# Kernel optimization log

Hardware: AMD Instinct MI355X
Metric: run time of the kernel (lower is better)

Reference implementation:

```python
import jax, jax.numpy as jnp
import numpy as np

B, S, D, H = 4, 1024, 256, 8  # batch, seq, d_model (== head_dim), n_heads
SCALE = 1.0 / float(np.sqrt(D))  # source references undefined self.scale; use 1/sqrt(d_model)


def setup_inputs() -> dict:
    key = jax.random.key(0)
    ks = jax.random.split(key, 11)
    w = 0.02
    return {
        "value_input": jax.random.normal(ks[0], (B, S, D), dtype=jnp.float32),
        "key_input": jax.random.normal(ks[1], (B, S, D), dtype=jnp.float32),
        "query_input": jax.random.normal(ks[2], (B, S, D), dtype=jnp.float32),
        "Wv": jax.random.normal(ks[3], (D, D * H), dtype=jnp.float32) * w,
        "bv": jnp.zeros((D * H,), dtype=jnp.float32),
        "Wk": jax.random.normal(ks[4], (D, D * H), dtype=jnp.float32) * w,
        "bk": jnp.zeros((D * H,), dtype=jnp.float32),
        "Wq": jax.random.normal(ks[5], (D, D * H), dtype=jnp.float32) * w,
        "bq": jnp.zeros((D * H,), dtype=jnp.float32),
        "Wo": jax.random.normal(ks[6], (D * H, D), dtype=jnp.float32) * w,
        "bo": jnp.zeros((D,), dtype=jnp.float32),
    }


def reference(value_input, key_input, query_input, Wv, bv, Wk, bk, Wq, bq, Wo, bo):
    # Fused QKV-style projections, then split into heads along last dim.
    # torch.split(..., d_model, dim=-1) == reshape to (B, S, H, D).
    v = (value_input @ Wv + bv).reshape(B, S, H, D)
    k = (key_input @ Wk + bk).reshape(B, S, H, D)
    q = (query_input @ Wq + bq).reshape(B, S, H, D)
    # Source: dot = k @ q^T  -> scores[b,h,key_pos,query_pos]
    scores = jnp.einsum('bkhd,bqhd->bhkq', k, q) * SCALE
    # Softmax over dim=-1 == the QUERY axis (faithful to source, nonstandard).
    attn = jax.nn.softmax(scores, axis=-1)
    # attn @ v : contract query axis with v's seq axis -> output indexed by key pos
    out_h = jnp.einsum('bhkq,bqhd->bkhd', attn, v)
    concat = out_h.reshape(B, S, H * D)
    return concat @ Wo + bo
```

## Files before the change

### kernel.cpp

```cpp
#include <hip/hip_runtime.h>
#include <cstddef>
#include <cstdint>

#define Bz 4
#define Sz 1024
#define Dm 256
#define Hh 8
#define DHh 2048
#define SCALE 0.0625f

typedef __attribute__((ext_vector_type(8))) short short8;
typedef __attribute__((ext_vector_type(16))) float f32x16;

__device__ inline unsigned short f2bf(float f){
  unsigned u = __float_as_uint(f);
  u += 0x7FFFu + ((u >> 16) & 1u);
  return (unsigned short)(u >> 16);
}
__device__ inline unsigned pk2(float a, float b){
  return (unsigned)f2bf(a) | ((unsigned)f2bf(b) << 16);
}
__device__ inline void gll16(const void* g, void* l){
  __builtin_amdgcn_global_load_lds((const __attribute__((address_space(1))) unsigned*)g,
                                   (__attribute__((address_space(3))) unsigned*)l, 16, 0, 0);
}
__device__ inline short8 lds8(const char* p){ return *(const short8*)p; }
__device__ inline f32x16 MM(short8 a, short8 b, f32x16 c){
  return __builtin_amdgcn_mfma_f32_32x32x16_bf16(a, b, c, 0, 0, 0);
}
__device__ inline f32x16 z16(){ f32x16 v; 
#pragma unroll
  for(int i=0;i<16;i++) v[i]=0.f; return v; }

__global__ __launch_bounds__(256) void cvt_bf16(const float* __restrict__ src,
                                                unsigned short* __restrict__ dst, int n4){
  int i = blockIdx.x*256 + threadIdx.x;
  if(i < n4){
    float4 v = ((const float4*)src)[i];
    ushort4 o; o.x=f2bf(v.x); o.y=f2bf(v.y); o.z=f2bf(v.z); o.w=f2bf(v.w);
    ((ushort4*)dst)[i] = o;
  }
}

__global__ __launch_bounds__(256) void cvt_transpose(const float* __restrict__ W,
    unsigned short* __restrict__ Wt, int K, int N){
  __shared__ float t[32][33];
  const int n0 = blockIdx.x*32, k0 = blockIdx.y*32;
  const int a = threadIdx.x >> 5, c = threadIdx.x & 31;
#pragma unroll
  for(int p=0;p<4;p++)
    t[a + p*8][c] = W[(size_t)(k0 + a + p*8)*N + n0 + c];
  __syncthreads();
#pragma unroll
  for(int p=0;p<4;p++)
    Wt[(size_t)(n0 + a + p*8)*K + k0 + c] = f2bf(t[c][a + p*8]);
}

template<int VAR>
__global__ __launch_bounds__(256) void gemm_proj(const unsigned short* __restrict__ A,
    const unsigned short* __restrict__ Bt, const float* __restrict__ bias,
    unsigned short* __restrict__ C){
  __shared__ __align__(16) char sm[32768];
  const int tid = threadIdx.x, w = tid>>6, lane = tid&63, l31 = lane&31, hp = lane>>5;
  const int wm = (w>>1)*64, wn = (w&1)*64;
  const int bm = blockIdx.y*128, bn = blockIdx.x*128;
  f32x16 acc[2][2]; acc[0][0]=z16(); acc[0][1]=z16(); acc[1][0]=z16(); acc[1][1]=z16();
  for(int kk=0; kk<256; kk+=64){
#pragma unroll
    for(int j=0;j<4;j++){
      int ci = (w*4+j)*64 + lane;
      int m = ci>>3, sl = ci&7;
      gll16(A  + (size_t)(bm+m)*256 + kk + ((sl ^ (m&7))<<3), sm + (w*4+j)*1024);
      gll16(Bt + (size_t)(bn+m)*256 + kk + ((sl ^ (m&7))<<3), sm + 16384 + (w*4+j)*1024);
    }
    __syncthreads();
#pragma unroll
    for(int s=0;s<4;s++){
      int m0 = wm + l31, m1 = wm + 32 + l31;
      int n0 = wn + l31, n1 = wn + 32 + l31;
      short8 a0 = lds8(sm + m0*128 + (((s*2+hp) ^ (m0&7))<<4));
      short8 a1 = lds8(sm + m1*128 + (((s*2+hp) ^ (m1&7))<<4));
      short8 b0 = lds8(sm + 16384 + n0*128 + (((s*2+hp) ^ (n0&7))<<4));
      short8 b1 = lds8(sm + 16384 + n1*128 + (((s*2+hp) ^ (n1&7))<<4));
      acc[0][0] = MM(a0,b0,acc[0][0]); acc[0][1] = MM(a0,b1,acc[0][1]);
      acc[1][0] = MM(a1,b0,acc[1][0]); acc[1][1] = MM(a1,b1,acc[1][1]);
    }
    __syncthreads();
  }
#pragma unroll
  for(int nh=0; nh<2; nh++){
    int ncol = bn + wn + nh*32 + l31;
    float bb = bias[ncol];
#pragma unroll
    for(int mh=0; mh<2; mh++){
      if(VAR == 2){
        int hidx = ncol >> 8, d = ncol & 255;
#pragma unroll
        for(int g=0; g<4; g++){
          int mrow = bm + wm + mh*32 + 8*g + 4*hp;
          int batch = mrow >> 10, sin = mrow & 1023;
          unsigned u0 = pk2(acc[mh][nh][4*g+0] + bb, acc[mh][nh][4*g+1] + bb);
          unsigned u1 = pk2(acc[mh][nh][4*g+2] + bb, acc[mh][nh][4*g+3] + bb);
          uint2 uu; uu.x = u0; uu.y = u1;
          *(uint2*)(C + ((size_t)((batch*Hh + hidx)*Dm + d))*Sz + sin) = uu;
        }
      } else {
#pragma unroll
        for(int r=0; r<16; r++){
          int mrow = bm + wm + mh*32 + (r&3) + 8*(r>>2) + 4*hp;
          float v = acc[mh][nh][r] + bb;
          if(VAR == 1) v *= SCALE;
          C[(size_t)mrow*DHh + ncol] = f2bf(v);
        }
      }
    }
  }
}

__global__ __launch_bounds__(512, 2) void attn_mfma(
    const unsigned short* __restrict__ Kp, const unsigned short* __restrict__ Qp,
    const unsigned short* __restrict__ Vt, unsigned short* __restrict__ Oc){
  __shared__ __align__(16) char sm[133120];
  const int tid = threadIdx.x, w = tid>>6, lane = tid&63, l31 = lane&31, hp = lane>>5;
  const int set = w>>2, ws = w&3;
  const int h = blockIdx.y, b = blockIdx.z;
  const int brow0 = blockIdx.x*128;
  const size_t vtbase = ((size_t)((b*Hh + h)*Dm))*Sz;

  short8 kp[16];
  {
    const unsigned short* kr = Kp + (size_t)(b*Sz + brow0 + ws*32 + l31)*DHh + h*Dm + hp*8;
#pragma unroll
    for(int ki=0; ki<16; ki++) kp[ki] = *(const short8*)(kr + ki*16);
  }
  f32x16 acc[8];
#pragma unroll
  for(int f=0; f<8; f++) acc[f] = z16();
  float m_run = -3.0e38f, l_run = 0.f;
  char* qpL = sm + set*16384;
  char* vtL = sm + 32768 + set*16384;

  for(int it=0; it<16; ++it){
    const int kv0 = set*512 + it*32;
#pragma unroll
    for(int j=0; j<4; j++){
      int ci = (ws*4+j)*64 + lane;
      int c = ci>>5, sl5 = ci&31;
      gll16(Qp + (size_t)(b*Sz + kv0 + c)*DHh + h*Dm + ((sl5 ^ (c&31))<<3),
            qpL + (ws*4+j)*1024);
      int dp = ci>>3, sv = (ci&7) ^ (dp&7);
      int d = dp*2 + (sv>>2), co = (sv&3)*8;
      gll16(Vt + vtbase + (size_t)d*Sz + kv0 + co, vtL + (ws*4+j)*1024);
    }
    __syncthreads();
    f32x16 S = z16();
#pragma unroll
    for(int ki=0; ki<16; ki++){
      short8 a = lds8(qpL + l31*512 + (((ki*2+hp) ^ (l31&31))<<4));
      S = MM(a, kp[ki], S);
    }
    float tmax = S[0];
#pragma unroll
    for(int r=1; r<16; r++) tmax = fmaxf(tmax, S[r]);
    tmax = fmaxf(tmax, __shfl_xor(tmax, 32));
    if(!__all(tmax <= m_run + 8.0f)){
      float mnew = fmaxf(m_run, tmax);
      float alpha = __expf(m_run - mnew);
      m_run = mnew; l_run *= alpha;
#pragma unroll
      for(int r=0; r<16; r++){
        int rr = (r&3) + 8*(r>>2) + 4*hp;
        float ar = __shfl(alpha, rr);
#pragma unroll
        for(int f=0; f<8; f++) acc[f][r] *= ar;
      }
    }
    float lsum = 0.f;
#pragma unroll
    for(int r=0; r<16; r++){ S[r] = __expf(S[r] - m_run); lsum += S[r]; }
    lsum += __shfl_xor(lsum, 32);
    l_run += lsum;
    short8 pa[2];
#pragma unroll
    for(int t=0; t<2; t++){
      unsigned w01 = pk2(S[t*8+0], S[t*8+1]);
      unsigned w23 = pk2(S[t*8+2], S[t*8+3]);
      unsigned w45 = pk2(S[t*8+4], S[t*8+5]);
      unsigned w67 = pk2(S[t*8+6], S[t*8+7]);
      unsigned x01 = __shfl_xor(w01, 32), x23 = __shfl_xor(w23, 32);
      unsigned x45 = __shfl_xor(w45, 32), x67 = __shfl_xor(w67, 32);
      union { unsigned u[4]; short8 s8; } U;
      if(hp == 0){ U.u[0]=w01; U.u[1]=w23; U.u[2]=x01; U.u[3]=x23; }
      else       { U.u[0]=x45; U.u[1]=x67; U.u[2]=w45; U.u[3]=w67; }
      pa[t] = U.s8;
    }
#pragma unroll
    for(int t=0; t<2; t++){
#pragma unroll
      for(int f=0; f<8; f++){
        int d = f*32 + l31;
        int dp = d>>1;
        int slot = (d&1)*4 + t*2 + hp;
        short8 vfr = lds8(vtL + dp*128 + ((slot ^ (dp&7))<<4));
        acc[f] = MM(pa[t], vfr, acc[f]);
      }
    }
    __syncthreads();
  }
  float* stats = (float*)(sm + 131072);
  if(lane < 32){ stats[(w*32 + lane)*2 + 0] = m_run; stats[(w*32 + lane)*2 + 1] = l_run; }
  __syncthreads();
  float* mg = (float*)sm + ws*8192;
  if(set == 1){
    float mA = stats[(ws*32 + l31)*2 + 0];
    float mf = fmaxf(mA, m_run);
    float bB = __expf(m_run - mf);
#pragma unroll
    for(int r=0; r<16; r++){
      int rr = (r&3) + 8*(r>>2) + 4*hp;
      float br = __shfl(bB, rr);
#pragma unroll
      for(int f=0; f<8; f++) mg[rr*256 + f*32 + l31] = acc[f][r]*br;
    }
  }
  __syncthreads();
  if(set == 0){
    float mB = stats[((4+ws)*32 + l31)*2 + 0];
    float lB = stats[((4+ws)*32 + l31)*2 + 1];
    float mf = fmaxf(m_run, mB);
    float bA = __expf(m_run - mf), bBv = __expf(mB - mf);
    float inv = 1.0f / (l_run*bA + lB*bBv);
#pragma unroll
    for(int r=0; r<16; r++){
      int rr = (r&3) + 8*(r>>2) + 4*hp;
      float bAr = __shfl(bA, rr);
      float invr = __shfl(inv, rr);
      int srow = brow0 + ws*32 + rr;
#pragma unroll
      for(int f=0; f<8; f++){
        float v = (acc[f][r]*bAr + mg[rr*256 + f*32 + l31]) * invr;
        Oc[(size_t)(b*Sz + srow)*DHh + h*Dm + f*32 + l31] = f2bf(v);
      }
    }
  }
}

__global__ __launch_bounds__(64) void gemm_out(const unsigned short* __restrict__ A,
    const unsigned short* __restrict__ Bt, const float* __restrict__ bias,
    float* __restrict__ C){
  __shared__ __align__(16) char sm[8192];
  const int lane = threadIdx.x, l31 = lane&31, hp = lane>>5;
  const int bm = blockIdx.y*32, bn = blockIdx.x*32;
  f32x16 acc = z16();
  for(int kk=0; kk<2048; kk+=64){
#pragma unroll
    for(int j=0; j<4; j++){
      int ci = j*64 + lane;
      int m = ci>>3, sl = ci&7;
      gll16(A  + (size_t)(bm+m)*DHh + kk + ((sl ^ (m&7))<<3), sm + j*1024);
      gll16(Bt + (size_t)(bn+m)*DHh + kk + ((sl ^ (m&7))<<3), sm + 4096 + j*1024);
    }
    __syncthreads();
#pragma unroll
    for(int s=0; s<4; s++){
      short8 a = lds8(sm + l31*128 + (((s*2+hp) ^ (l31&7))<<4));
      short8 b = lds8(sm + 4096 + l31*128 + (((s*2+hp) ^ (l31&7))<<4));
      acc = MM(a, b, acc);
    }
    __syncthreads();
  }
  float bb = bias[bn + l31];
#pragma unroll
  for(int r=0; r<16; r++){
    int mrow = bm + (r&3) + 8*(r>>2) + 4*hp;
    C[(size_t)mrow*Dm + bn + l31] = acc[r] + bb;
  }
}

extern "C" void kernel_launch(void* const* d_in, const int* in_sizes, int n_in,
                              void* d_out, int out_size, void* d_ws, size_t ws_size,
                              hipStream_t stream){
  (void)in_sizes; (void)n_in; (void)out_size; (void)ws_size;
  const float* value_in = (const float*)d_in[0];
  const float* key_in   = (const float*)d_in[1];
  const float* query_in = (const float*)d_in[2];
  const float* Wv = (const float*)d_in[3];
  const float* bv = (const float*)d_in[4];
  const float* Wk = (const float*)d_in[5];
  const float* bk = (const float*)d_in[6];
  const float* Wq = (const float*)d_in[7];
  const float* bq = (const float*)d_in[8];
  const float* Wo = (const float*)d_in[9];
  const float* bo = (const float*)d_in[10];

  char* ws = (char*)d_ws;
  unsigned short* av  = (unsigned short*)(ws + ((size_t) 0u<<20));
  unsigned short* ak  = (unsigned short*)(ws + ((size_t) 2u<<20));
  unsigned short* aq  = (unsigned short*)(ws + ((size_t) 4u<<20));
  unsigned short* wtv = (unsigned short*)(ws + ((size_t) 6u<<20));
  unsigned short* wtk = (unsigned short*)(ws + ((size_t) 7u<<20));
  unsigned short* wtq = (unsigned short*)(ws + ((size_t) 8u<<20));
  unsigned short* wto = (unsigned short*)(ws + ((size_t) 9u<<20));
  unsigned short* vt  = (unsigned short*)(ws + ((size_t)10u<<20));
  unsigned short* kb  = (unsigned short*)(ws + ((size_t)26u<<20));
  unsigned short* qb  = (unsigned short*)(ws + ((size_t)42u<<20));
  unsigned short* cc  = (unsigned short*)(ws + ((size_t)58u<<20));

  cvt_bf16<<<1024, 256, 0, stream>>>(value_in, av, 262144);
  cvt_bf16<<<1024, 256, 0, stream>>>(key_in,   ak, 262144);
  cvt_bf16<<<1024, 256, 0, stream>>>(query_in, aq, 262144);
  cvt_transpose<<<dim3(64, 8), 256, 0, stream>>>(Wv, wtv, 256, 2048);
  cvt_transpose<<<dim3(64, 8), 256, 0, stream>>>(Wk, wtk, 256, 2048);
  cvt_transpose<<<dim3(64, 8), 256, 0, stream>>>(Wq, wtq, 256, 2048);
  cvt_transpose<<<dim3(8, 64), 256, 0, stream>>>(Wo, wto, 2048, 256);

  gemm_proj<2><<<dim3(16, 32), 256, 0, stream>>>(av, wtv, bv, vt);
  gemm_proj<1><<<dim3(16, 32), 256, 0, stream>>>(ak, wtk, bk, kb);
  gemm_proj<0><<<dim3(16, 32), 256, 0, stream>>>(aq, wtq, bq, qb);

  attn_mfma<<<dim3(8, Hh, Bz), 512, 0, stream>>>(kb, qb, vt, cc);

  gemm_out<<<dim3(8, 128), 64, 0, stream>>>(cc, wto, bo, (float*)d_out);
}
```

Measured before the change: 251.3 us.

## Double-buffer LDS in GEMMs and attention, merge convert launches, retile output GEMM

```diff
diff --git a/kernel.cpp b/kernel.cpp
--- a/kernel.cpp
+++ b/kernel.cpp
@@ -28,24 +28,36 @@
 __device__ inline f32x16 MM(short8 a, short8 b, f32x16 c){
   return __builtin_amdgcn_mfma_f32_32x32x16_bf16(a, b, c, 0, 0, 0);
 }
-__device__ inline f32x16 z16(){ f32x16 v; 
+__device__ inline f32x16 z16(){ f32x16 v;
 #pragma unroll
   for(int i=0;i<16;i++) v[i]=0.f; return v; }
 
-__global__ __launch_bounds__(256) void cvt_bf16(const float* __restrict__ src,
-                                                unsigned short* __restrict__ dst, int n4){
-  int i = blockIdx.x*256 + threadIdx.x;
-  if(i < n4){
-    float4 v = ((const float4*)src)[i];
-    ushort4 o; o.x=f2bf(v.x); o.y=f2bf(v.y); o.z=f2bf(v.z); o.w=f2bf(v.w);
-    ((ushort4*)dst)[i] = o;
-  }
-}
-
-__global__ __launch_bounds__(256) void cvt_transpose(const float* __restrict__ W,
-    unsigned short* __restrict__ Wt, int K, int N){
+__global__ __launch_bounds__(256) void cvt_a(
+    const float* __restrict__ S0, const float* __restrict__ S1, const float* __restrict__ S2,
+    unsigned short* __restrict__ D0, unsigned short* __restrict__ D1, unsigned short* __restrict__ D2){
+  const int bx = blockIdx.x;
+  const int seg = bx >> 10;
+  const float* src = seg==0 ? S0 : seg==1 ? S1 : S2;
+  unsigned short* dst = seg==0 ? D0 : seg==1 ? D1 : D2;
+  const int i = (bx & 1023)*256 + threadIdx.x;
+  float4 v = ((const float4*)src)[i];
+  ushort4 o; o.x=f2bf(v.x); o.y=f2bf(v.y); o.z=f2bf(v.z); o.w=f2bf(v.w);
+  ((ushort4*)dst)[i] = o;
+}
+
+__global__ __launch_bounds__(256) void cvt_w(
+    const float* __restrict__ W0, const float* __restrict__ W1,
+    const float* __restrict__ W2, const float* __restrict__ W3,
+    unsigned short* __restrict__ T0, unsigned short* __restrict__ T1,
+    unsigned short* __restrict__ T2, unsigned short* __restrict__ T3){
   __shared__ float t[32][33];
-  const int n0 = blockIdx.x*32, k0 = blockIdx.y*32;
+  const int z = blockIdx.z;
+  const float* W = z==0 ? W0 : z==1 ? W1 : z==2 ? W2 : W3;
+  unsigned short* T = z==0 ? T0 : z==1 ? T1 : z==2 ? T2 : T3;
+  const int K = (z<3) ? 256 : 2048;
+  const int N = (z<3) ? 2048 : 256;
+  const int n0 = (z<3) ? blockIdx.x*32 : blockIdx.y*32;
+  const int k0 = (z<3) ? blockIdx.y*32 : blockIdx.x*32;
   const int a = threadIdx.x >> 5, c = threadIdx.x & 31;
 #pragma unroll
   for(int p=0;p<4;p++)
@@ -53,39 +65,48 @@
   __syncthreads();
 #pragma unroll
   for(int p=0;p<4;p++)
-    Wt[(size_t)(n0 + a + p*8)*K + k0 + c] = f2bf(t[c][a + p*8]);
+    T[(size_t)(n0 + a + p*8)*K + k0 + c] = f2bf(t[c][a + p*8]);
 }
 
 template<int VAR>
 __global__ __launch_bounds__(256) void gemm_proj(const unsigned short* __restrict__ A,
     const unsigned short* __restrict__ Bt, const float* __restrict__ bias,
     unsigned short* __restrict__ C){
-  __shared__ __align__(16) char sm[32768];
+  __shared__ __align__(16) char sm[65536];
   const int tid = threadIdx.x, w = tid>>6, lane = tid&63, l31 = lane&31, hp = lane>>5;
   const int wm = (w>>1)*64, wn = (w&1)*64;
   const int bm = blockIdx.y*128, bn = blockIdx.x*128;
   f32x16 acc[2][2]; acc[0][0]=z16(); acc[0][1]=z16(); acc[1][0]=z16(); acc[1][1]=z16();
-  for(int kk=0; kk<256; kk+=64){
+
+  auto STAGE = [&](int db, int kk){
 #pragma unroll
     for(int j=0;j<4;j++){
       int ci = (w*4+j)*64 + lane;
       int m = ci>>3, sl = ci&7;
-      gll16(A  + (size_t)(bm+m)*256 + kk + ((sl ^ (m&7))<<3), sm + (w*4+j)*1024);
-      gll16(Bt + (size_t)(bn+m)*256 + kk + ((sl ^ (m&7))<<3), sm + 16384 + (w*4+j)*1024);
-    }
-    __syncthreads();
+      gll16(A  + (size_t)(bm+m)*256 + kk + ((sl ^ (m&7))<<3), sm + db*32768 + (w*4+j)*1024);
+      gll16(Bt + (size_t)(bn+m)*256 + kk + ((sl ^ (m&7))<<3), sm + db*32768 + 16384 + (w*4+j)*1024);
+    }
+  };
+
+  STAGE(0, 0);
+  __syncthreads();
+  int db = 0;
+  for(int t=0; t<4; ++t){
+    if(t<3) STAGE(db^1, (t+1)*64);
+    const char* base = sm + db*32768;
 #pragma unroll
     for(int s=0;s<4;s++){
       int m0 = wm + l31, m1 = wm + 32 + l31;
       int n0 = wn + l31, n1 = wn + 32 + l31;
-      short8 a0 = lds8(sm + m0*128 + (((s*2+hp) ^ (m0&7))<<4));
-      short8 a1 = lds8(sm + m1*128 + (((s*2+hp) ^ (m1&7))<<4));
-      short8 b0 = lds8(sm + 16384 + n0*128 + (((s*2+hp) ^ (n0&7))<<4));
-      short8 b1 = lds8(sm + 16384 + n1*128 + (((s*2+hp) ^ (n1&7))<<4));
+      short8 a0 = lds8(base + m0*128 + (((s*2+hp) ^ (m0&7))<<4));
+      short8 a1 = lds8(base + m1*128 + (((s*2+hp) ^ (m1&7))<<4));
+      short8 b0 = lds8(base + 16384 + n0*128 + (((s*2+hp) ^ (n0&7))<<4));
+      short8 b1 = lds8(base + 16384 + n1*128 + (((s*2+hp) ^ (n1&7))<<4));
       acc[0][0] = MM(a0,b0,acc[0][0]); acc[0][1] = MM(a0,b1,acc[0][1]);
       acc[1][0] = MM(a1,b0,acc[1][0]); acc[1][1] = MM(a1,b1,acc[1][1]);
     }
     __syncthreads();
+    db ^= 1;
   }
 #pragma unroll
   for(int nh=0; nh<2; nh++){
@@ -123,8 +144,10 @@
   __shared__ __align__(16) char sm[133120];
   const int tid = threadIdx.x, w = tid>>6, lane = tid&63, l31 = lane&31, hp = lane>>5;
   const int set = w>>2, ws = w&3;
-  const int h = blockIdx.y, b = blockIdx.z;
-  const int brow0 = blockIdx.x*128;
+  const int bid = blockIdx.x;
+  const int g = (bid & 7)*4 + (bid >> 6);
+  const int b = g >> 3, h = g & 7;
+  const int brow0 = ((bid >> 3) & 7) * 128;
   const size_t vtbase = ((size_t)((b*Hh + h)*Dm))*Sz;
 
   short8 kp[16];
@@ -137,26 +160,34 @@
 #pragma unroll
   for(int f=0; f<8; f++) acc[f] = z16();
   float m_run = -3.0e38f, l_run = 0.f;
-  char* qpL = sm + set*16384;
-  char* vtL = sm + 32768 + set*16384;
-
-  for(int it=0; it<16; ++it){
+
+  auto STAGE = [&](int db, int it){
     const int kv0 = set*512 + it*32;
+    char* qpD = sm + db*65536 + set*16384;
+    char* vtD = sm + db*65536 + 32768 + set*16384;
 #pragma unroll
     for(int j=0; j<4; j++){
       int ci = (ws*4+j)*64 + lane;
       int c = ci>>5, sl5 = ci&31;
-      gll16(Qp + (size_t)(b*Sz + kv0 + c)*DHh + h*Dm + ((sl5 ^ (c&31))<<3),
-            qpL + (ws*4+j)*1024);
+      gll16(Qp + (size_t)(b*Sz + kv0 + c)*DHh + h*Dm + ((sl5 ^ c)<<3),
+            qpD + (ws*4+j)*1024);
       int dp = ci>>3, sv = (ci&7) ^ (dp&7);
       int d = dp*2 + (sv>>2), co = (sv&3)*8;
-      gll16(Vt + vtbase + (size_t)d*Sz + kv0 + co, vtL + (ws*4+j)*1024);
-    }
-    __syncthreads();
+      gll16(Vt + vtbase + (size_t)d*Sz + kv0 + co, vtD + (ws*4+j)*1024);
+    }
+  };
+
+  STAGE(0, 0);
+  __syncthreads();
+  int db = 0;
+  for(int it=0; it<16; ++it){
+    if(it<15) STAGE(db^1, it+1);
+    const char* qpL = sm + db*65536 + set*16384;
+    const char* vtL = sm + db*65536 + 32768 + set*16384;
     f32x16 S = z16();
 #pragma unroll
     for(int ki=0; ki<16; ki++){
-      short8 a = lds8(qpL + l31*512 + (((ki*2+hp) ^ (l31&31))<<4));
+      short8 a = lds8(qpL + l31*512 + (((ki*2+hp) ^ l31)<<4));
       S = MM(a, kp[ki], S);
     }
     float tmax = S[0];
@@ -206,6 +237,7 @@
       }
     }
     __syncthreads();
+    db ^= 1;
   }
   float* stats = (float*)(sm + 131072);
   if(lane < 32){ stats[(w*32 + lane)*2 + 0] = m_run; stats[(w*32 + lane)*2 + 1] = l_run; }
@@ -245,35 +277,46 @@
   }
 }
 
-__global__ __launch_bounds__(64) void gemm_out(const unsigned short* __restrict__ A,
+__global__ __launch_bounds__(256) void gemm_out(const unsigned short* __restrict__ A,
     const unsigned short* __restrict__ Bt, const float* __restrict__ bias,
     float* __restrict__ C){
-  __shared__ __align__(16) char sm[8192];
-  const int lane = threadIdx.x, l31 = lane&31, hp = lane>>5;
-  const int bm = blockIdx.y*32, bn = blockIdx.x*32;
+  __shared__ __align__(16) char sm[32768];
+  const int tid = threadIdx.x, w = tid>>6, lane = tid&63, l31 = lane&31, hp = lane>>5;
+  const int wm = (w>>1)*32, wn = (w&1)*32;
+  const int bm = blockIdx.y*64, bn = blockIdx.x*64;
   f32x16 acc = z16();
-  for(int kk=0; kk<2048; kk+=64){
-#pragma unroll
-    for(int j=0; j<4; j++){
-      int ci = j*64 + lane;
+
+  auto STAGE = [&](int db, int kk){
+#pragma unroll
+    for(int j=0; j<2; j++){
+      int ci = (w*2+j)*64 + lane;
       int m = ci>>3, sl = ci&7;
-      gll16(A  + (size_t)(bm+m)*DHh + kk + ((sl ^ (m&7))<<3), sm + j*1024);
-      gll16(Bt + (size_t)(bn+m)*DHh + kk + ((sl ^ (m&7))<<3), sm + 4096 + j*1024);
+      gll16(A  + (size_t)(bm+m)*DHh + kk + ((sl ^ (m&7))<<3), sm + db*16384 + (w*2+j)*1024);
+      gll16(Bt + (size_t)(bn+m)*DHh + kk + ((sl ^ (m&7))<<3), sm + db*16384 + 8192 + (w*2+j)*1024);
+    }
+  };
+
+  STAGE(0, 0);
+  __syncthreads();
+  int db = 0;
+  for(int t=0; t<32; ++t){
+    if(t<31) STAGE(db^1, (t+1)*64);
+    const char* base = sm + db*16384;
+#pragma unroll
+    for(int s=0; s<4; s++){
+      int m0 = wm + l31, n0 = wn + l31;
+      short8 a = lds8(base + m0*128 + (((s*2+hp) ^ (m0&7))<<4));
+      short8 b = lds8(base + 8192 + n0*128 + (((s*2+hp) ^ (n0&7))<<4));
+      acc = MM(a, b, acc);
     }
     __syncthreads();
-#pragma unroll
-    for(int s=0; s<4; s++){
-      short8 a = lds8(sm + l31*128 + (((s*2+hp) ^ (l31&7))<<4));
-      short8 b = lds8(sm + 4096 + l31*128 + (((s*2+hp) ^ (l31&7))<<4));
-      acc = MM(a, b, acc);
-    }
-    __syncthreads();
-  }
-  float bb = bias[bn + l31];
+    db ^= 1;
+  }
+  float bb = bias[bn + wn + l31];
 #pragma unroll
   for(int r=0; r<16; r++){
-    int mrow = bm + (r&3) + 8*(r>>2) + 4*hp;
-    C[(size_t)mrow*Dm + bn + l31] = acc[r] + bb;
+    int mrow = bm + wm + (r&3) + 8*(r>>2) + 4*hp;
+    C[(size_t)mrow*Dm + bn + wn + l31] = acc[r] + bb;
   }
 }
 
@@ -306,19 +349,14 @@
   unsigned short* qb  = (unsigned short*)(ws + ((size_t)42u<<20));
   unsigned short* cc  = (unsigned short*)(ws + ((size_t)58u<<20));
 
-  cvt_bf16<<<1024, 256, 0, stream>>>(value_in, av, 262144);
-  cvt_bf16<<<1024, 256, 0, stream>>>(key_in,   ak, 262144);
-  cvt_bf16<<<1024, 256, 0, stream>>>(query_in, aq, 262144);
-  cvt_transpose<<<dim3(64, 8), 256, 0, stream>>>(Wv, wtv, 256, 2048);
-  cvt_transpose<<<dim3(64, 8), 256, 0, stream>>>(Wk, wtk, 256, 2048);
-  cvt_transpose<<<dim3(64, 8), 256, 0, stream>>>(Wq, wtq, 256, 2048);
-  cvt_transpose<<<dim3(8, 64), 256, 0, stream>>>(Wo, wto, 2048, 256);
+  cvt_a<<<3072, 256, 0, stream>>>(value_in, key_in, query_in, av, ak, aq);
+  cvt_w<<<dim3(64, 8, 4), 256, 0, stream>>>(Wv, Wk, Wq, Wo, wtv, wtk, wtq, wto);
 
   gemm_proj<2><<<dim3(16, 32), 256, 0, stream>>>(av, wtv, bv, vt);
   gemm_proj<1><<<dim3(16, 32), 256, 0, stream>>>(ak, wtk, bk, kb);
   gemm_proj<0><<<dim3(16, 32), 256, 0, stream>>>(aq, wtq, bq, qb);
 
-  attn_mfma<<<dim3(8, Hh, Bz), 512, 0, stream>>>(kb, qb, vt, cc);
-
-  gemm_out<<<dim3(8, 128), 64, 0, stream>>>(cc, wto, bo, (float*)d_out);
-}
+  attn_mfma<<<256, 512, 0, stream>>>(kb, qb, vt, cc);
+
+  gemm_out<<<dim3(4, 64), 256, 0, stream>>>(cc, wto, bo, (float*)d_out);
+}
```

Result: faster. 208.2 us (-17.2%).
